# Optimization experiments

Hardware: AMD Instinct MI355X
Metric: run time of the kernel (lower is better)

Reference implementation:

```python
import jax, jax.numpy as jnp
import numpy as np
import itertools, math

# ---- config (mirrors args in init_kwargs) ----
BS = 8
FRAME_H, FRAME_W = 120, 160
RES = 5            # map_resolution (cm/cell)
Z_RES = 5
MAP_SIZE_CM = 2400
VR = 100           # vision_range (cells)
FOV = 79.0
NSEM = 16
CAT_THR, EXP_THR, MAP_THR = 5.0, 1.0, 1.0
CAM_H_CM = 88.0    # camera_height * 100
MAX_H = int(360 / Z_RES)   # 72
MIN_H = int(-40 / Z_RES)   # -8
D = MAX_H - MIN_H          # 80
MAP_SZ = MAP_SIZE_CM // RES  # 480
C = 4 + NSEM
XC = (FRAME_W - 1.0) / 2.0
ZC = (FRAME_H - 1.0) / 2.0
F_CAM = (FRAME_W / 2.0) / math.tan(math.radians(FOV / 2.0))


def splat_feat_nd(feat, coords, grid_dims):
    # feat: [B, nF, nPt], coords: [B, 3, nPt] in [-1, 1]; trilinear scatter-add
    B, nF, nPt = feat.shape
    pos_dim, wts_dim = [], []
    for d, gd in enumerate(grid_dims):
        pos = coords[:, d, :] * (gd / 2.0) + gd / 2.0
        fl = jnp.floor(pos)
        pd, wd = [], []
        for ix in (0.0, 1.0):
            p = fl + ix
            safe = ((p > 0) & (p < gd)).astype(pos.dtype)
            wd.append((1.0 - jnp.abs(pos - p)) * safe)
            pd.append(p * safe)
        pos_dim.append(pd)
        wts_dim.append(wd)
    T = grid_dims[0] * grid_dims[1] * grid_dims[2]
    idxs, wts = [], []
    for ix_d in itertools.product((0, 1), (0, 1), (0, 1)):
        index = jnp.zeros_like(pos_dim[0][0])
        w = jnp.ones_like(index)
        for d in range(3):
            index = index * grid_dims[d] + pos_dim[d][ix_d[d]]
            w = w * wts_dim[d][ix_d[d]]
        idxs.append(index.astype(jnp.int32))
        wts.append(w)
    idx = jnp.concatenate(idxs, axis=-1)              # [B, 8*nPt]
    w = jnp.concatenate(wts, axis=-1)                 # [B, 8*nPt]
    src = jnp.tile(feat, (1, 1, 8)) * w[:, None, :]   # [B, nF, 8*nPt]

    def scat(src_b, idx_b):
        return jnp.zeros((nF, T), src_b.dtype).at[:, idx_b].add(src_b)

    grid = jax.vmap(scat)(src, idx)
    grid = jnp.clip(grid, 0.0, 1e3)
    return grid.reshape(B, nF, grid_dims[0], grid_dims[1], grid_dims[2])


def _base_grid(N, dtype):
    # torch affine_grid default align_corners=False pixel-center coords
    c = (2.0 * jnp.arange(N, dtype=dtype) + 1.0) / N - 1.0
    x = jnp.broadcast_to(c[None, :], (N, N))
    y = jnp.broadcast_to(c[:, None], (N, N))
    return x, y


def affine_grid_rot(t_deg, N):
    t = t_deg * (np.pi / 180.0)
    ct, st = jnp.cos(t), jnp.sin(t)
    x, y = _base_grid(N, t.dtype)
    gx = ct[:, None, None] * x - st[:, None, None] * y
    gy = st[:, None, None] * x + ct[:, None, None] * y
    return jnp.stack([gx, gy], -1)


def affine_grid_trans(xy, N):
    x, y = _base_grid(N, xy.dtype)
    gx = x[None] + xy[:, 0][:, None, None]
    gy = y[None] + xy[:, 1][:, None, None]
    return jnp.stack([gx, gy], -1)


def grid_sample(im, grid):
    # bilinear, align_corners=True, padding_mode='zeros'
    B, Ch, H, W = im.shape
    x = (grid[..., 0] + 1.0) * 0.5 * (W - 1)
    y = (grid[..., 1] + 1.0) * 0.5 * (H - 1)
    x0 = jnp.floor(x); y0 = jnp.floor(y)
    x1 = x0 + 1.0; y1 = y0 + 1.0

    def gather(im_b, iy, ix):
        valid = (ix >= 0) & (ix < W) & (iy >= 0) & (iy < H)
        ixc = jnp.clip(ix, 0, W - 1).astype(jnp.int32)
        iyc = jnp.clip(iy, 0, H - 1).astype(jnp.int32)
        return im_b[:, iyc, ixc] * valid[None].astype(im_b.dtype)

    def sample_one(im_b, x, y, x0, x1, y0, y1):
        wa = (x1 - x) * (y1 - y); wb = (x1 - x) * (y - y0)
        wc = (x - x0) * (y1 - y); wd = (x - x0) * (y - y0)
        return (gather(im_b, y0, x0) * wa[None] + gather(im_b, y1, x0) * wb[None]
                + gather(im_b, y0, x1) * wc[None] + gather(im_b, y1, x1) * wd[None])

    return jax.vmap(sample_one)(im, x, y, x0, x1, y0, y1)


def setup_inputs() -> dict:
    key = jax.random.key(0)
    k1, k2, k3, k4, k5, k6 = jax.random.split(key, 6)
    rgb = jax.random.uniform(k1, (BS, 3, FRAME_H, FRAME_W), jnp.float32)
    depth = jax.random.uniform(k2, (BS, 1, FRAME_H, FRAME_W), jnp.float32, 0.5, 5.0)
    sem = jax.random.uniform(k3, (BS, NSEM, FRAME_H, FRAME_W), jnp.float32)
    obs = jnp.concatenate([rgb, depth, sem], axis=1)
    maps_last = jax.random.uniform(k4, (BS, C, MAP_SZ, MAP_SZ), jnp.float32)
    xy = jax.random.uniform(k5, (BS, 2), jnp.float32, 2.0, 22.0)
    th = jax.random.uniform(k6, (BS, 1), jnp.float32, 0.0, 360.0)
    poses = jnp.concatenate([xy, th], axis=1)
    return {"obs": obs, "maps_last": maps_last, "poses": poses}


def reference(obs, maps_last, poses):
    bs = obs.shape[0]
    depth = obs[:, 3]
    rowmax = jnp.max(depth, axis=(0, 2))  # per image-row max over batch+width
    depth = jnp.where(depth == 0.0, rowmax[None, :, None], depth) * 100.0
    # point cloud from depth (du_scale=1)
    gx = jnp.arange(FRAME_W, dtype=depth.dtype)                 # column index
    gz = jnp.arange(FRAME_H - 1, -1, -1, dtype=depth.dtype)     # flipped row index
    X = (gx[None, None, :] - XC) * depth / F_CAM
    Z = (gz[None, :, None] - ZC) * depth / F_CAM
    Y = depth
    # camera -> agent frame (elev=0 -> identity rot), then shift_loc (theta=pi/2 -> identity rot)
    X = X + (VR * RES // 2)
    Z = Z + CAM_H_CM
    # normalize to [-1, 1] voxel coords
    xs = (X / RES - VR // 2.0) / VR * 2.0
    ys = (Y / RES - VR // 2.0) / VR * 2.0
    zs = (Z / Z_RES - (MAX_H + MIN_H) // 2.0) / (MAX_H - MIN_H) * 2.0
    coords = jnp.stack([xs, ys, zs], axis=1).reshape(bs, 3, -1)   # [B,3,nPt]
    feat = jnp.concatenate(
        [jnp.ones((bs, 1, FRAME_H * FRAME_W), obs.dtype),
         obs[:, 4:].reshape(bs, NSEM, -1)], axis=1)               # [B,1+NSEM,nPt]
    voxels = splat_feat_nd(feat, coords, (VR, VR, D))
    voxels = jnp.swapaxes(voxels, 2, 3)
    min_z = int(25 / Z_RES - MIN_H)                 # 13
    max_z = int((CAM_H_CM + 1) / Z_RES - MIN_H)     # 25
    agent_hp = voxels[..., min_z:max_z].sum(4)
    all_hp = voxels.sum(4)
    fp_map = jnp.clip(agent_hp[:, 0:1] / MAP_THR, 0.0, 1.0)
    fp_exp = jnp.clip(all_hp[:, 0:1] / EXP_THR, 0.0, 1.0)
    cat_pred = jnp.clip(agent_hp[:, 1:] / CAT_THR, 0.0, 1.0)
    x1 = MAP_SZ // 2 - VR // 2; x2 = x1 + VR
    y1 = MAP_SZ // 2; y2 = y1 + VR
    agent_view = jnp.zeros((bs, C, MAP_SZ, MAP_SZ), obs.dtype)
    agent_view = agent_view.at[:, 0:1, y1:y2, x1:x2].set(fp_map)
    agent_view = agent_view.at[:, 1:2, y1:y2, x1:x2].set(fp_exp)
    agent_view = agent_view.at[:, 4:4 + NSEM, y1:y2, x1:x2].set(cat_pred)
    # st_pose (detached in original)
    p = jax.lax.stop_gradient(poses)
    half = MAP_SZ // 2
    st_xy = -(p[:, :2] * 100.0 / RES - half) / half
    st_t = 90.0 - p[:, 2]
    rotated = grid_sample(agent_view, affine_grid_rot(st_t, MAP_SZ))
    translated = grid_sample(rotated, affine_grid_trans(st_xy, MAP_SZ))
    map_pred = jnp.maximum(maps_last, translated)
    map_pred = map_pred.at[:, 2].set(map_pred[:, 3])
    curr = (p[:, :2] * 100.0 / RES).astype(jnp.int32)
    rr = curr[:, 1]; cc = curr[:, 0]
    ii = jnp.arange(MAP_SZ)
    mask = (jnp.abs(ii[None, :, None] - rr[:, None, None]) <= 1) & \
           (jnp.abs(ii[None, None, :] - cc[:, None, None]) <= 1)
    map_pred = map_pred.at[:, 3].set(jnp.where(mask, 1.0, map_pred[:, 3]))
    return map_pred
```

## Files before the change

### kernel.cpp

```cpp
#include <hip/hip_runtime.h>
#include <hip/hip_bf16.h>
#include <math.h>

#define FRAME_W 160
#define FRAME_H 120
#define NPIX (FRAME_W*FRAME_H)
#define BS_ 8
#define CC_ 20
#define MAPSZ 480
#define MPIX (MAPSZ*MAPSZ)
#define AVC 18
#define AV_ELEMS ((size_t)BS_*100*100*AVC)
#define ROT0 120
#define ROT1 360

#define STRIP_H 4
#define NSTRIP 25
#define SPLAT_T 1024
#define TILE_ELEMS (STRIP_H*100*AVC)

template<bool BF>
__device__ __forceinline__ float ldv(const void* p, size_t i){
    if constexpr (BF) return __bfloat162float(((const __hip_bfloat16*)p)[i]);
    else              return ((const float*)p)[i];
}
template<bool BF>
__device__ __forceinline__ void stv(void* p, size_t i, float v){
    if constexpr (BF) ((__hip_bfloat16*)p)[i] = __float2bfloat16(v);
    else              ((float*)p)[i] = v;
}
template<bool BF>
__device__ __forceinline__ void ld2v(const void* p, size_t i, float& a, float& b){
    if constexpr (BF){
        ushort2 u = ((const ushort2*)p)[i>>1];
        a = __uint_as_float((unsigned)u.x << 16);
        b = __uint_as_float((unsigned)u.y << 16);
    } else {
        float2 v = ((const float2*)p)[i>>1];
        a = v.x; b = v.y;
    }
}
template<bool BF>
__device__ __forceinline__ void st2v(void* p, size_t i, float a, float b){
    if constexpr (BF){
        __hip_bfloat162 h;
        h.x = __float2bfloat16(a); h.y = __float2bfloat16(b);
        ((__hip_bfloat162*)p)[i>>1] = h;
    } else {
        ((float2*)p)[i>>1] = make_float2(a, b);
    }
}

extern "C" __global__ void smk75806v6_detect(const void* __restrict__ poses,
                                             int* __restrict__ flag,
                                             float* __restrict__ params)
{
    if (threadIdx.x == 0 && blockIdx.x == 0){
        const __hip_bfloat16* pb = (const __hip_bfloat16*)poses;
        int ok = 1;
        for (int k = 0; k < 24; k++){
            float v = __bfloat162float(pb[k]);
            if (!(v >= 0.0f && v < 400.0f)) ok = 0;
        }
        *flag = ok;
        for (int b = 0; b < BS_; b++){
            float p0, p1, th;
            if (ok){
                p0 = __bfloat162float(pb[b*3+0]);
                p1 = __bfloat162float(pb[b*3+1]);
                th = __bfloat162float(pb[b*3+2]);
            } else {
                const float* pf = (const float*)poses;
                p0 = pf[b*3+0]; p1 = pf[b*3+1]; th = pf[b*3+2];
            }
            params[b*8+0] = -((p0*100.0f/5.0f) - 240.0f)/240.0f;
            params[b*8+1] = -((p1*100.0f/5.0f) - 240.0f)/240.0f;
            float t = (90.0f - th) * 0.017453292519943295f;
            params[b*8+2] = cosf(t);
            params[b*8+3] = sinf(t);
            params[b*8+4] = p1*100.0f/5.0f;
            params[b*8+5] = p0*100.0f/5.0f;
        }
    }
}

template<bool BF>
__device__ __forceinline__ void splat_strip_impl(const void* __restrict__ obs,
                                                 float* __restrict__ av,
                                                 float* __restrict__ tile,
                                                 int b, int y0)
{
    const int tid = threadIdx.x;
    const size_t ob = (size_t)b*CC_*NPIX;
    const float f_cam = (float)(80.0 / tan(0.6894050545377601));

    for (int k = tid; k < TILE_ELEMS/4; k += SPLAT_T)
        ((float4*)tile)[k] = make_float4(0.f,0.f,0.f,0.f);
    __syncthreads();

    const int NQ = NPIX/4;
    for (int qp = tid; qp < NQ; qp += SPLAT_T){
        float d4[4];
        if constexpr (BF){
            ushort4 u = ((const ushort4*)((const __hip_bfloat16*)obs + ob + 3*NPIX))[qp];
            d4[0] = __uint_as_float((unsigned)u.x << 16);
            d4[1] = __uint_as_float((unsigned)u.y << 16);
            d4[2] = __uint_as_float((unsigned)u.z << 16);
            d4[3] = __uint_as_float((unsigned)u.w << 16);
        } else {
            float4 v = ((const float4*)((const float*)obs + ob + 3*NPIX))[qp];
            d4[0]=v.x; d4[1]=v.y; d4[2]=v.z; d4[3]=v.w;
        }
        #pragma unroll
        for (int u=0;u<4;u++){
            int pix = qp*4 + u;
            float d100 = d4[u] * 100.0f;

            float ys   = (d100/5.0f - 50.0f)/100.0f*2.0f;
            float posy = ys*50.0f + 50.0f;
            float fly  = floorf(posy);
            int   ify  = (int)fly;
            if (ify < y0 - 1 || ify > y0 + STRIP_H - 1) continue;

            int r = pix / FRAME_W, c = pix - r*FRAME_W;
            float X = ((float)c - 79.5f) * d100 / f_cam + 250.0f;
            float Z = ((float)(FRAME_H-1 - r) - 59.5f) * d100 / f_cam + 88.0f;
            float xs = (X/5.0f - 50.0f)/100.0f*2.0f;
            float zs = (Z/5.0f - 32.0f)/80.0f*2.0f;
            float posx = xs*50.0f + 50.0f;
            float posz = zs*40.0f + 40.0f;

            float flx = floorf(posx), flz = floorf(posz);
            float wx[2], wy[2]; int ixv[2], iyv[2]; bool own[2];
            #pragma unroll
            for (int k=0;k<2;k++){
                float px = flx + (float)k;
                wx[k] = (px > 0.0f && px < 100.0f) ? (1.0f - fabsf(posx - px)) : 0.0f;
                ixv[k] = (int)px;
                float py = fly + (float)k;
                bool valid = (py > 0.0f && py < 100.0f);
                wy[k] = valid ? (1.0f - fabsf(posy - py)) : 0.0f;
                iyv[k] = (int)py;
                own[k] = valid && (iyv[k] >= y0) && (iyv[k] < y0 + STRIP_H);
            }
            if (!own[0] && !own[1]) continue;

            float wzall = 0.0f, wzag = 0.0f;
            #pragma unroll
            for (int k=0;k<2;k++){
                float pz = flz + (float)k;
                if (pz > 0.0f && pz < 80.0f){
                    float w = 1.0f - fabsf(posz - pz);
                    wzall += w;
                    int ipz = (int)pz;
                    if (ipz >= 13 && ipz < 25) wzag += w;
                }
            }
            if (wzall == 0.0f) continue;

            float sem[16];
            bool needsem = (wzag != 0.0f);
            if (needsem){
                #pragma unroll
                for (int s=0;s<16;s++) sem[s] = ldv<BF>(obs, ob + (size_t)(4+s)*NPIX + pix);
            }

            #pragma unroll
            for (int ky=0;ky<2;ky++){
                if (!own[ky] || wy[ky] == 0.0f) continue;
                #pragma unroll
                for (int kx=0;kx<2;kx++){
                    float wxy = wx[kx]*wy[ky];
                    if (wxy == 0.0f) continue;
                    float* cell = tile + (((iyv[ky]-y0)*100 + ixv[kx])*AVC);
                    atomicAdd(cell + 0, wxy*wzall);
                    float wa = wxy*wzag;
                    if (wa != 0.0f){
                        atomicAdd(cell + 1, wa);
                        #pragma unroll
                        for (int s=0;s<16;s++) atomicAdd(cell + 2 + s, wa*sem[s]);
                    }
                }
            }
        }
    }

    __syncthreads();
    size_t gbase4 = ((size_t)b*100 + y0)*(size_t)(100*AVC) / 4;
    for (int k = tid; k < TILE_ELEMS/4; k += SPLAT_T)
        ((float4*)av)[gbase4 + k] = ((const float4*)tile)[k];
}

extern "C" __global__ __launch_bounds__(SPLAT_T)
void smk75806v6_splat(const void* __restrict__ obs, float* __restrict__ av,
                      const int* __restrict__ flag)
{
    __shared__ float tile[TILE_ELEMS];
    int bid = blockIdx.x;
    int b  = bid & 7;
    int y0 = (bid >> 3) * STRIP_H;
    if (*flag) splat_strip_impl<true >(obs, av, tile, b, y0);
    else       splat_strip_impl<false>(obs, av, tile, b, y0);
}

template<bool BF>
__device__ __forceinline__ void final_impl(const float* __restrict__ av,
                                           const void* __restrict__ maps_last,
                                           const float* __restrict__ params,
                                           void* __restrict__ out, int gid)
{
    int b = gid / (MPIX/2);
    int rem = gid - b*(MPIX/2);
    int i  = rem / (MAPSZ/2);
    int j0 = (rem - i*(MAPSZ/2))*2;

    const float* pb = params + b*8;
    float tx = pb[0], ty = pb[1], ct = pb[2], st = pb[3];
    int rr = (int)pb[4];
    int cc = (int)pb[5];

    size_t mlb = (size_t)b*CC_*MPIX;
    size_t px  = (size_t)i*MAPSZ + j0;

    float m0a,m0b, m1a,m1b, m3a,m3b;
    ld2v<BF>(maps_last, mlb + 0*MPIX + px, m0a, m0b);
    ld2v<BF>(maps_last, mlb + 1*MPIX + px, m1a, m1b);
    ld2v<BF>(maps_last, mlb + 3*MPIX + px, m3a, m3b);

    float acc[2][18];
    #pragma unroll
    for (int u=0;u<2;u++)
        #pragma unroll
        for (int q=0;q<18;q++) acc[u][q]=0.0f;

    float yb = (2.0f*(float)i + 1.0f)/480.0f - 1.0f + ty;
    float y = (yb + 1.0f)*0.5f*479.0f;
    float y0f = floorf(y);
    int y0 = (int)y0f;
    float wyv[2] = {(y0f + 1.0f) - y, y - y0f};

    #pragma unroll
    for (int u=0;u<2;u++){
        int j = j0 + u;
        float xb = (2.0f*(float)j + 1.0f)/480.0f - 1.0f + tx;
        float x = (xb + 1.0f)*0.5f*479.0f;
        float x0f = floorf(x);
        int x0 = (int)x0f;
        float wxv[2] = {(x0f + 1.0f) - x, x - x0f};

        if (x0+1 >= ROT0 && x0 < ROT1 && y0+1 >= ROT0 && y0 < ROT1){
            #pragma unroll
            for (int ty2=0;ty2<2;ty2++){
                #pragma unroll
                for (int tx2=0;tx2<2;tx2++){
                    int yy = y0 + ty2, xx = x0 + tx2;
                    float w = wxv[tx2]*wyv[ty2];
                    if (w == 0.0f) continue;
                    if (yy < ROT0 || yy >= ROT1 || xx < ROT0 || xx >= ROT1) continue;
                    float xb2 = (2.0f*(float)xx + 1.0f)/480.0f - 1.0f;
                    float yb2 = (2.0f*(float)yy + 1.0f)/480.0f - 1.0f;
                    float gx = ct*xb2 - st*yb2;
                    float gy = st*xb2 + ct*yb2;
                    float x2 = (gx + 1.0f)*0.5f*479.0f;
                    float y2 = (gy + 1.0f)*0.5f*479.0f;
                    float x20f = floorf(x2), y20f = floorf(y2);
                    int x20 = (int)x20f, y20 = (int)y20f;
                    float wx2[2] = {(x20f + 1.0f) - x2, x2 - x20f};
                    float wy2[2] = {(y20f + 1.0f) - y2, y2 - y20f};

                    float rs[18];
                    #pragma unroll
                    for (int q=0;q<18;q++) rs[q]=0.0f;
                    #pragma unroll
                    for (int sy=0;sy<2;sy++){
                        #pragma unroll
                        for (int sx=0;sx<2;sx++){
                            int ay = y20 + sy, ax = x20 + sx;
                            float w2 = wx2[sx]*wy2[sy];
                            if (w2 == 0.0f) continue;
                            if (ay < 240 || ay >= 340 || ax < 190 || ax >= 290) continue;
                            const float* cell = av + (((size_t)b*100 + (ay-240))*100 + (ax-190))*AVC;
                            rs[0] += w2 * fminf(cell[1], 1.0f);
                            rs[1] += w2 * fminf(cell[0], 1.0f);
                            #pragma unroll
                            for (int s=0;s<16;s++)
                                rs[2+s] += w2 * fminf(cell[2+s]*0.2f, 1.0f);
                        }
                    }
                    #pragma unroll
                    for (int q=0;q<18;q++) acc[u][q] += w*rs[q];
                }
            }
        }
    }

    bool m3u0 = ((i - rr) <= 1 && (rr - i) <= 1) && ((j0   - cc) <= 1 && (cc - j0  ) <= 1);
    bool m3u1 = ((i - rr) <= 1 && (rr - i) <= 1) && ((j0+1 - cc) <= 1 && (cc - j0-1) <= 1);

    float f3a = fmaxf(m3a, 0.0f);
    float f3b = fmaxf(m3b, 0.0f);
    st2v<BF>(out, mlb + 0*MPIX + px, fmaxf(m0a, acc[0][0]), fmaxf(m0b, acc[1][0]));
    st2v<BF>(out, mlb + 1*MPIX + px, fmaxf(m1a, acc[0][1]), fmaxf(m1b, acc[1][1]));
    st2v<BF>(out, mlb + 2*MPIX + px, f3a, f3b);
    st2v<BF>(out, mlb + 3*MPIX + px, m3u0 ? 1.0f : f3a, m3u1 ? 1.0f : f3b);

    float sa[16], sb[16];
    #pragma unroll
    for (int q=0;q<16;q++)
        ld2v<BF>(maps_last, mlb + (size_t)(4+q)*MPIX + px, sa[q], sb[q]);
    #pragma unroll
    for (int q=0;q<16;q++)
        st2v<BF>(out, mlb + (size_t)(4+q)*MPIX + px,
                 fmaxf(sa[q], acc[0][2+q]), fmaxf(sb[q], acc[1][2+q]));
}

extern "C" __global__ __launch_bounds__(256)
void smk75806v6_final(const float* __restrict__ av,
                      const void* __restrict__ maps_last,
                      const float* __restrict__ params,
                      void* __restrict__ out,
                      const int* __restrict__ flag)
{
    int gid = blockIdx.x*256 + threadIdx.x;
    if (gid >= BS_*MPIX/2) return;
    if (*flag) final_impl<true >(av, maps_last, params, out, gid);
    else       final_impl<false>(av, maps_last, params, out, gid);
}

extern "C" void kernel_launch(void* const* d_in, const int* in_sizes, int n_in,
                              void* d_out, int out_size, void* d_ws, size_t ws_size,
                              hipStream_t stream) {
    const void* pO = d_in[0];
    const void* pM = (n_in > 1) ? d_in[1] : d_in[0];
    const void* pP = (n_in > 2) ? d_in[2] : d_in[0];
    for (int i = 0; i < n_in; i++){
        if      (in_sizes[i] == BS_*CC_*NPIX) pO = d_in[i];
        else if (in_sizes[i] == BS_*CC_*MPIX) pM = d_in[i];
        else if (in_sizes[i] == BS_*3)        pP = d_in[i];
    }
    int*   flag   = (int*)d_ws;
    float* params = (float*)((char*)d_ws + 64);
    float* av     = (float*)((char*)d_ws + 512);

    smk75806v6_detect<<<1, 64, 0, stream>>>(pP, flag, params);
    smk75806v6_splat <<<BS_*NSTRIP, SPLAT_T, 0, stream>>>(pO, av, flag);
    smk75806v6_final <<<(BS_*MPIX/2 + 255)/256, 256, 0, stream>>>(av, pM, params, d_out, flag);
}
```

Before: 340.5 us.

## Precompute rotated map into workspace buffer and fold detect kernel into splat

Splits the fused rotate+translate sampling into two passes. A new kernel materializes the rotated 18-channel map over the 240x240 region into a planar workspace buffer, and the final kernel then does a single bilinear lookup per pixel instead of recomputing the rotation sample for each of four neighbors. The splatted map is now stored channel-planar, the pose detect/params kernel is folded into the splat kernel, and the final kernel handles one pixel per thread. This adds a kernel launch and about 33 MB of intermediate traffic, and falls back to the old fused path when the workspace is too small.

```diff
diff --git a/kernel.cpp b/kernel.cpp
--- a/kernel.cpp
+++ b/kernel.cpp
@@ -10,9 +10,14 @@
 #define MAPSZ 480
 #define MPIX (MAPSZ*MAPSZ)
 #define AVC 18
-#define AV_ELEMS ((size_t)BS_*100*100*AVC)
+#define AVP 10000
 #define ROT0 120
 #define ROT1 360
+#define RW   240
+#define RPTS (RW*RW)
+#define WS_AV_OFF   512
+#define WS_R_OFF    (6*1024*1024)
+#define WS_NEED     ((size_t)WS_R_OFF + (size_t)BS_*AVC*RPTS*4)
 
 #define STRIP_H 4
 #define NSTRIP 25
@@ -29,59 +34,16 @@
     if constexpr (BF) ((__hip_bfloat16*)p)[i] = __float2bfloat16(v);
     else              ((float*)p)[i] = v;
 }
-template<bool BF>
-__device__ __forceinline__ void ld2v(const void* p, size_t i, float& a, float& b){
-    if constexpr (BF){
-        ushort2 u = ((const ushort2*)p)[i>>1];
-        a = __uint_as_float((unsigned)u.x << 16);
-        b = __uint_as_float((unsigned)u.y << 16);
-    } else {
-        float2 v = ((const float2*)p)[i>>1];
-        a = v.x; b = v.y;
-    }
-}
-template<bool BF>
-__device__ __forceinline__ void st2v(void* p, size_t i, float a, float b){
-    if constexpr (BF){
-        __hip_bfloat162 h;
-        h.x = __float2bfloat16(a); h.y = __float2bfloat16(b);
-        ((__hip_bfloat162*)p)[i>>1] = h;
-    } else {
-        ((float2*)p)[i>>1] = make_float2(a, b);
-    }
-}
-
-extern "C" __global__ void smk75806v6_detect(const void* __restrict__ poses,
-                                             int* __restrict__ flag,
-                                             float* __restrict__ params)
-{
-    if (threadIdx.x == 0 && blockIdx.x == 0){
-        const __hip_bfloat16* pb = (const __hip_bfloat16*)poses;
-        int ok = 1;
-        for (int k = 0; k < 24; k++){
-            float v = __bfloat162float(pb[k]);
-            if (!(v >= 0.0f && v < 400.0f)) ok = 0;
-        }
-        *flag = ok;
-        for (int b = 0; b < BS_; b++){
-            float p0, p1, th;
-            if (ok){
-                p0 = __bfloat162float(pb[b*3+0]);
-                p1 = __bfloat162float(pb[b*3+1]);
-                th = __bfloat162float(pb[b*3+2]);
-            } else {
-                const float* pf = (const float*)poses;
-                p0 = pf[b*3+0]; p1 = pf[b*3+1]; th = pf[b*3+2];
-            }
-            params[b*8+0] = -((p0*100.0f/5.0f) - 240.0f)/240.0f;
-            params[b*8+1] = -((p1*100.0f/5.0f) - 240.0f)/240.0f;
-            float t = (90.0f - th) * 0.017453292519943295f;
-            params[b*8+2] = cosf(t);
-            params[b*8+3] = sinf(t);
-            params[b*8+4] = p1*100.0f/5.0f;
-            params[b*8+5] = p0*100.0f/5.0f;
-        }
-    }
+
+__device__ __forceinline__ int detect_flag(const void* poses){
+    const __hip_bfloat16* pb = (const __hip_bfloat16*)poses;
+    int ok = 1;
+    #pragma unroll
+    for (int k = 0; k < 24; k++){
+        float v = __bfloat162float(pb[k]);
+        if (!(v >= 0.0f && v < 400.0f)) ok = 0;
+    }
+    return ok;
 }
 
 template<bool BF>
@@ -93,10 +55,6 @@
     const int tid = threadIdx.x;
     const size_t ob = (size_t)b*CC_*NPIX;
     const float f_cam = (float)(80.0 / tan(0.6894050545377601));
-
-    for (int k = tid; k < TILE_ELEMS/4; k += SPLAT_T)
-        ((float4*)tile)[k] = make_float4(0.f,0.f,0.f,0.f);
-    __syncthreads();
 
     const int NQ = NPIX/4;
     for (int qp = tid; qp < NQ; qp += SPLAT_T){
@@ -186,145 +144,302 @@
     }
 
     __syncthreads();
-    size_t gbase4 = ((size_t)b*100 + y0)*(size_t)(100*AVC) / 4;
+    for (int k = tid; k < TILE_ELEMS; k += SPLAT_T){
+        int ch = k / 400;
+        int rc = k - ch*400;
+        av[((size_t)b*AVC + ch)*AVP + y0*100 + rc] = tile[rc*AVC + ch];
+    }
+}
+
+extern "C" __global__ __launch_bounds__(SPLAT_T)
+void smk75806v7_splat(const void* __restrict__ obs,
+                      const void* __restrict__ poses,
+                      float* __restrict__ av,
+                      int* __restrict__ flag,
+                      float* __restrict__ params)
+{
+    __shared__ float tile[TILE_ELEMS];
+    __shared__ int sflag;
+    int tid = threadIdx.x;
+
+    if (tid < 8){
+        int ok = detect_flag(poses);
+        if (tid == 0) sflag = ok;
+        if (blockIdx.x == 0){
+            if (tid == 0) *flag = ok;
+            int b = tid;
+            float p0, p1, th;
+            if (ok){
+                const __hip_bfloat16* pb = (const __hip_bfloat16*)poses;
+                p0 = __bfloat162float(pb[b*3+0]);
+                p1 = __bfloat162float(pb[b*3+1]);
+                th = __bfloat162float(pb[b*3+2]);
+            } else {
+                const float* pf = (const float*)poses;
+                p0 = pf[b*3+0]; p1 = pf[b*3+1]; th = pf[b*3+2];
+            }
+            params[b*8+0] = -((p0*100.0f/5.0f) - 240.0f)/240.0f;
+            params[b*8+1] = -((p1*100.0f/5.0f) - 240.0f)/240.0f;
+            float t = (90.0f - th) * 0.017453292519943295f;
+            params[b*8+2] = cosf(t);
+            params[b*8+3] = sinf(t);
+            params[b*8+4] = p1*100.0f/5.0f;
+            params[b*8+5] = p0*100.0f/5.0f;
+        }
+    }
     for (int k = tid; k < TILE_ELEMS/4; k += SPLAT_T)
-        ((float4*)av)[gbase4 + k] = ((const float4*)tile)[k];
-}
-
-extern "C" __global__ __launch_bounds__(SPLAT_T)
-void smk75806v6_splat(const void* __restrict__ obs, float* __restrict__ av,
-                      const int* __restrict__ flag)
-{
-    __shared__ float tile[TILE_ELEMS];
+        ((float4*)tile)[k] = make_float4(0.f,0.f,0.f,0.f);
+    __syncthreads();
+
     int bid = blockIdx.x;
     int b  = bid & 7;
     int y0 = (bid >> 3) * STRIP_H;
-    if (*flag) splat_strip_impl<true >(obs, av, tile, b, y0);
+    if (sflag) splat_strip_impl<true >(obs, av, tile, b, y0);
     else       splat_strip_impl<false>(obs, av, tile, b, y0);
 }
 
+extern "C" __global__ __launch_bounds__(256)
+void smk75806v7_rot(const float* __restrict__ av,
+                    const float* __restrict__ params,
+                    float* __restrict__ R)
+{
+    int gid = blockIdx.x*256 + threadIdx.x;
+    if (gid >= BS_*RPTS) return;
+    int b = gid / RPTS;
+    int rem = gid - b*RPTS;
+    int ry = rem / RW, rx = rem - ry*RW;
+    int yy = ry + ROT0, xx = rx + ROT0;
+
+    float ct = params[b*8+2], st = params[b*8+3];
+    float xb2 = (2.0f*(float)xx + 1.0f)/480.0f - 1.0f;
+    float yb2 = (2.0f*(float)yy + 1.0f)/480.0f - 1.0f;
+    float gx = ct*xb2 - st*yb2;
+    float gy = st*xb2 + ct*yb2;
+    float x2 = (gx + 1.0f)*0.5f*479.0f;
+    float y2 = (gy + 1.0f)*0.5f*479.0f;
+    float x20f = floorf(x2), y20f = floorf(y2);
+    int x20 = (int)x20f, y20 = (int)y20f;
+    float wx2[2] = {(x20f + 1.0f) - x2, x2 - x20f};
+    float wy2[2] = {(y20f + 1.0f) - y2, y2 - y20f};
+
+    float wf[4]; int off[4]; bool any = false;
+    #pragma unroll
+    for (int t=0;t<4;t++){
+        int sy = t>>1, sx = t&1;
+        int ay = y20 + sy, ax = x20 + sx;
+        float w2 = wx2[sx]*wy2[sy];
+        bool v = (ay >= 240 && ay < 340 && ax >= 190 && ax < 290) && (w2 != 0.0f);
+        wf[t]  = v ? w2 : 0.0f;
+        off[t] = v ? (ay-240)*100 + (ax-190) : 0;
+        any |= v;
+    }
+
+    float* Rb = R + (size_t)b*AVC*RPTS + rem;
+    if (!any){
+        #pragma unroll
+        for (int q=0;q<AVC;q++) Rb[(size_t)q*RPTS] = 0.0f;
+        return;
+    }
+    const float* avb = av + (size_t)b*AVC*AVP;
+    #pragma unroll
+    for (int q=0;q<AVC;q++){
+        int pl = (q==0) ? 1 : ((q==1) ? 0 : q);
+        float sc = (q>=2) ? 0.2f : 1.0f;
+        const float* ap = avb + (size_t)pl*AVP;
+        float v = wf[0]*fminf(ap[off[0]]*sc, 1.0f)
+                + wf[1]*fminf(ap[off[1]]*sc, 1.0f)
+                + wf[2]*fminf(ap[off[2]]*sc, 1.0f)
+                + wf[3]*fminf(ap[off[3]]*sc, 1.0f);
+        Rb[(size_t)q*RPTS] = v;
+    }
+}
+
 template<bool BF>
-__device__ __forceinline__ void final_impl(const float* __restrict__ av,
-                                           const void* __restrict__ maps_last,
-                                           const float* __restrict__ params,
-                                           void* __restrict__ out, int gid)
-{
-    int b = gid / (MPIX/2);
-    int rem = gid - b*(MPIX/2);
-    int i  = rem / (MAPSZ/2);
-    int j0 = (rem - i*(MAPSZ/2))*2;
-
-    const float* pb = params + b*8;
-    float tx = pb[0], ty = pb[1], ct = pb[2], st = pb[3];
-    int rr = (int)pb[4];
-    int cc = (int)pb[5];
+__device__ __forceinline__ void finalB_impl(const float* __restrict__ R,
+                                            const void* __restrict__ maps_last,
+                                            const float* __restrict__ params,
+                                            void* __restrict__ out, int gid)
+{
+    int b = gid / MPIX;
+    int rem = gid - b*MPIX;
+    int i = rem / MAPSZ, j = rem - i*MAPSZ;
+
+    const float* pbp = params + b*8;
+    float tx = pbp[0], ty = pbp[1];
+    int rr = (int)pbp[4];
+    int cc = (int)pbp[5];
 
     size_t mlb = (size_t)b*CC_*MPIX;
-    size_t px  = (size_t)i*MAPSZ + j0;
-
-    float m0a,m0b, m1a,m1b, m3a,m3b;
-    ld2v<BF>(maps_last, mlb + 0*MPIX + px, m0a, m0b);
-    ld2v<BF>(maps_last, mlb + 1*MPIX + px, m1a, m1b);
-    ld2v<BF>(maps_last, mlb + 3*MPIX + px, m3a, m3b);
-
-    float acc[2][18];
-    #pragma unroll
-    for (int u=0;u<2;u++)
-        #pragma unroll
-        for (int q=0;q<18;q++) acc[u][q]=0.0f;
+    size_t px  = (size_t)rem;
+
+    float m0 = ldv<BF>(maps_last, mlb + 0*MPIX + px);
+    float m1 = ldv<BF>(maps_last, mlb + 1*MPIX + px);
+    float m3 = ldv<BF>(maps_last, mlb + 3*MPIX + px);
+    float ms[16];
+    #pragma unroll
+    for (int q=0;q<16;q++) ms[q] = ldv<BF>(maps_last, mlb + (size_t)(4+q)*MPIX + px);
+
+    float acc[18];
+    #pragma unroll
+    for (int q=0;q<18;q++) acc[q] = 0.0f;
 
     float yb = (2.0f*(float)i + 1.0f)/480.0f - 1.0f + ty;
     float y = (yb + 1.0f)*0.5f*479.0f;
-    float y0f = floorf(y);
-    int y0 = (int)y0f;
+    float xb = (2.0f*(float)j + 1.0f)/480.0f - 1.0f + tx;
+    float x = (xb + 1.0f)*0.5f*479.0f;
+    float x0f = floorf(x), y0f = floorf(y);
+    int x0 = (int)x0f, y0 = (int)y0f;
+    float wxv[2] = {(x0f + 1.0f) - x, x - x0f};
     float wyv[2] = {(y0f + 1.0f) - y, y - y0f};
 
-    #pragma unroll
-    for (int u=0;u<2;u++){
-        int j = j0 + u;
-        float xb = (2.0f*(float)j + 1.0f)/480.0f - 1.0f + tx;
-        float x = (xb + 1.0f)*0.5f*479.0f;
-        float x0f = floorf(x);
-        int x0 = (int)x0f;
-        float wxv[2] = {(x0f + 1.0f) - x, x - x0f};
-
-        if (x0+1 >= ROT0 && x0 < ROT1 && y0+1 >= ROT0 && y0 < ROT1){
+    if (x0+1 >= ROT0 && x0 < ROT1 && y0+1 >= ROT0 && y0 < ROT1){
+        float cw[4]; int coff[4];
+        #pragma unroll
+        for (int t=0;t<4;t++){
+            int ty2 = t>>1, tx2 = t&1;
+            int yy = y0 + ty2, xx = x0 + tx2;
+            float w = wxv[tx2]*wyv[ty2];
+            bool v = (yy >= ROT0 && yy < ROT1 && xx >= ROT0 && xx < ROT1);
+            cw[t]  = v ? w : 0.0f;
+            coff[t] = v ? (yy-ROT0)*RW + (xx-ROT0) : 0;
+        }
+        const float* Rb = R + (size_t)b*AVC*RPTS;
+        #pragma unroll
+        for (int q=0;q<18;q++){
+            const float* Rp = Rb + (size_t)q*RPTS;
+            acc[q] = cw[0]*Rp[coff[0]] + cw[1]*Rp[coff[1]]
+                   + cw[2]*Rp[coff[2]] + cw[3]*Rp[coff[3]];
+        }
+    }
+
+    bool m3m = (i - rr) <= 1 && (rr - i) <= 1 && (j - cc) <= 1 && (cc - j) <= 1;
+    float f3 = fmaxf(m3, 0.0f);
+    stv<BF>(out, mlb + 0*MPIX + px, fmaxf(m0, acc[0]));
+    stv<BF>(out, mlb + 1*MPIX + px, fmaxf(m1, acc[1]));
+    stv<BF>(out, mlb + 2*MPIX + px, f3);
+    stv<BF>(out, mlb + 3*MPIX + px, m3m ? 1.0f : f3);
+    #pragma unroll
+    for (int q=0;q<16;q++)
+        stv<BF>(out, mlb + (size_t)(4+q)*MPIX + px, fmaxf(ms[q], acc[2+q]));
+}
+
+extern "C" __global__ __launch_bounds__(256)
+void smk75806v7_finalB(const float* __restrict__ R,
+                       const void* __restrict__ maps_last,
+                       const float* __restrict__ params,
+                       void* __restrict__ out,
+                       const int* __restrict__ flag)
+{
+    int gid = blockIdx.x*256 + threadIdx.x;
+    if (gid >= BS_*MPIX) return;
+    if (*flag) finalB_impl<true >(R, maps_last, params, out, gid);
+    else       finalB_impl<false>(R, maps_last, params, out, gid);
+}
+
+template<bool BF>
+__device__ __forceinline__ void finalF_impl(const float* __restrict__ av,
+                                            const void* __restrict__ maps_last,
+                                            const float* __restrict__ params,
+                                            void* __restrict__ out, int gid)
+{
+    int b = gid / MPIX;
+    int rem = gid - b*MPIX;
+    int i = rem / MAPSZ, j = rem - i*MAPSZ;
+
+    const float* pbp = params + b*8;
+    float tx = pbp[0], ty = pbp[1], ct = pbp[2], st = pbp[3];
+    int rr = (int)pbp[4];
+    int cc = (int)pbp[5];
+
+    size_t mlb = (size_t)b*CC_*MPIX;
+    size_t px  = (size_t)rem;
+
+    float m0 = ldv<BF>(maps_last, mlb + 0*MPIX + px);
+    float m1 = ldv<BF>(maps_last, mlb + 1*MPIX + px);
+    float m3 = ldv<BF>(maps_last, mlb + 3*MPIX + px);
+
+    float acc[18];
+    #pragma unroll
+    for (int q=0;q<18;q++) acc[q]=0.0f;
+
+    float yb = (2.0f*(float)i + 1.0f)/480.0f - 1.0f + ty;
+    float y = (yb + 1.0f)*0.5f*479.0f;
+    float xb = (2.0f*(float)j + 1.0f)/480.0f - 1.0f + tx;
+    float x = (xb + 1.0f)*0.5f*479.0f;
+    float x0f = floorf(x), y0f = floorf(y);
+    int x0 = (int)x0f, y0 = (int)y0f;
+    float wxv[2] = {(x0f + 1.0f) - x, x - x0f};
+    float wyv[2] = {(y0f + 1.0f) - y, y - y0f};
+
+    if (x0+1 >= ROT0 && x0 < ROT1 && y0+1 >= ROT0 && y0 < ROT1){
+        #pragma unroll
+        for (int ty2=0;ty2<2;ty2++){
             #pragma unroll
-            for (int ty2=0;ty2<2;ty2++){
+            for (int tx2=0;tx2<2;tx2++){
+                int yy = y0 + ty2, xx = x0 + tx2;
+                float w = wxv[tx2]*wyv[ty2];
+                if (w == 0.0f) continue;
+                if (yy < ROT0 || yy >= ROT1 || xx < ROT0 || xx >= ROT1) continue;
+                float xb2 = (2.0f*(float)xx + 1.0f)/480.0f - 1.0f;
+                float yb2 = (2.0f*(float)yy + 1.0f)/480.0f - 1.0f;
+                float gx = ct*xb2 - st*yb2;
+                float gy = st*xb2 + ct*yb2;
+                float x2 = (gx + 1.0f)*0.5f*479.0f;
+                float y2 = (gy + 1.0f)*0.5f*479.0f;
+                float x20f = floorf(x2), y20f = floorf(y2);
+                int x20 = (int)x20f, y20 = (int)y20f;
+                float wx2[2] = {(x20f + 1.0f) - x2, x2 - x20f};
+                float wy2[2] = {(y20f + 1.0f) - y2, y2 - y20f};
+
+                float rs[18];
                 #pragma unroll
-                for (int tx2=0;tx2<2;tx2++){
-                    int yy = y0 + ty2, xx = x0 + tx2;
-                    float w = wxv[tx2]*wyv[ty2];
-                    if (w == 0.0f) continue;
-                    if (yy < ROT0 || yy >= ROT1 || xx < ROT0 || xx >= ROT1) continue;
-                    float xb2 = (2.0f*(float)xx + 1.0f)/480.0f - 1.0f;
-                    float yb2 = (2.0f*(float)yy + 1.0f)/480.0f - 1.0f;
-                    float gx = ct*xb2 - st*yb2;
-                    float gy = st*xb2 + ct*yb2;
-                    float x2 = (gx + 1.0f)*0.5f*479.0f;
-                    float y2 = (gy + 1.0f)*0.5f*479.0f;
-                    float x20f = floorf(x2), y20f = floorf(y2);
-                    int x20 = (int)x20f, y20 = (int)y20f;
-                    float wx2[2] = {(x20f + 1.0f) - x2, x2 - x20f};
-                    float wy2[2] = {(y20f + 1.0f) - y2, y2 - y20f};
-
-                    float rs[18];
+                for (int q=0;q<18;q++) rs[q]=0.0f;
+                #pragma unroll
+                for (int sy=0;sy<2;sy++){
                     #pragma unroll
-                    for (int q=0;q<18;q++) rs[q]=0.0f;
-                    #pragma unroll
-                    for (int sy=0;sy<2;sy++){
+                    for (int sx=0;sx<2;sx++){
+                        int ay = y20 + sy, ax = x20 + sx;
+                        float w2 = wx2[sx]*wy2[sy];
+                        if (w2 == 0.0f) continue;
+                        if (ay < 240 || ay >= 340 || ax < 190 || ax >= 290) continue;
+                        const float* cb = av + (size_t)b*AVC*AVP + (ay-240)*100 + (ax-190);
+                        rs[0] += w2 * fminf(cb[1*AVP], 1.0f);
+                        rs[1] += w2 * fminf(cb[0],     1.0f);
                         #pragma unroll
-                        for (int sx=0;sx<2;sx++){
-                            int ay = y20 + sy, ax = x20 + sx;
-                            float w2 = wx2[sx]*wy2[sy];
-                            if (w2 == 0.0f) continue;
-                            if (ay < 240 || ay >= 340 || ax < 190 || ax >= 290) continue;
-                            const float* cell = av + (((size_t)b*100 + (ay-240))*100 + (ax-190))*AVC;
-                            rs[0] += w2 * fminf(cell[1], 1.0f);
-                            rs[1] += w2 * fminf(cell[0], 1.0f);
-                            #pragma unroll
-                            for (int s=0;s<16;s++)
-                                rs[2+s] += w2 * fminf(cell[2+s]*0.2f, 1.0f);
-                        }
+                        for (int s=0;s<16;s++)
+                            rs[2+s] += w2 * fminf(cb[(size_t)(2+s)*AVP]*0.2f, 1.0f);
                     }
-                    #pragma unroll
-                    for (int q=0;q<18;q++) acc[u][q] += w*rs[q];
                 }
-            }
-        }
-    }
-
-    bool m3u0 = ((i - rr) <= 1 && (rr - i) <= 1) && ((j0   - cc) <= 1 && (cc - j0  ) <= 1);
-    bool m3u1 = ((i - rr) <= 1 && (rr - i) <= 1) && ((j0+1 - cc) <= 1 && (cc - j0-1) <= 1);
-
-    float f3a = fmaxf(m3a, 0.0f);
-    float f3b = fmaxf(m3b, 0.0f);
-    st2v<BF>(out, mlb + 0*MPIX + px, fmaxf(m0a, acc[0][0]), fmaxf(m0b, acc[1][0]));
-    st2v<BF>(out, mlb + 1*MPIX + px, fmaxf(m1a, acc[0][1]), fmaxf(m1b, acc[1][1]));
-    st2v<BF>(out, mlb + 2*MPIX + px, f3a, f3b);
-    st2v<BF>(out, mlb + 3*MPIX + px, m3u0 ? 1.0f : f3a, m3u1 ? 1.0f : f3b);
-
-    float sa[16], sb[16];
-    #pragma unroll
-    for (int q=0;q<16;q++)
-        ld2v<BF>(maps_last, mlb + (size_t)(4+q)*MPIX + px, sa[q], sb[q]);
-    #pragma unroll
-    for (int q=0;q<16;q++)
-        st2v<BF>(out, mlb + (size_t)(4+q)*MPIX + px,
-                 fmaxf(sa[q], acc[0][2+q]), fmaxf(sb[q], acc[1][2+q]));
+                #pragma unroll
+                for (int q=0;q<18;q++) acc[q] += w*rs[q];
+            }
+        }
+    }
+
+    bool m3m = (i - rr) <= 1 && (rr - i) <= 1 && (j - cc) <= 1 && (cc - j) <= 1;
+    float f3 = fmaxf(m3, 0.0f);
+    stv<BF>(out, mlb + 0*MPIX + px, fmaxf(m0, acc[0]));
+    stv<BF>(out, mlb + 1*MPIX + px, fmaxf(m1, acc[1]));
+    stv<BF>(out, mlb + 2*MPIX + px, f3);
+    stv<BF>(out, mlb + 3*MPIX + px, m3m ? 1.0f : f3);
+    #pragma unroll
+    for (int q=0;q<16;q++){
+        float v = fmaxf(ldv<BF>(maps_last, mlb + (size_t)(4+q)*MPIX + px), acc[2+q]);
+        stv<BF>(out, mlb + (size_t)(4+q)*MPIX + px, v);
+    }
 }
 
 extern "C" __global__ __launch_bounds__(256)
-void smk75806v6_final(const float* __restrict__ av,
-                      const void* __restrict__ maps_last,
-                      const float* __restrict__ params,
-                      void* __restrict__ out,
-                      const int* __restrict__ flag)
+void smk75806v7_finalF(const float* __restrict__ av,
+                       const void* __restrict__ maps_last,
+                       const float* __restrict__ params,
+                       void* __restrict__ out,
+                       const int* __restrict__ flag)
 {
     int gid = blockIdx.x*256 + threadIdx.x;
-    if (gid >= BS_*MPIX/2) return;
-    if (*flag) final_impl<true >(av, maps_last, params, out, gid);
-    else       final_impl<false>(av, maps_last, params, out, gid);
+    if (gid >= BS_*MPIX) return;
+    if (*flag) finalF_impl<true >(av, maps_last, params, out, gid);
+    else       finalF_impl<false>(av, maps_last, params, out, gid);
 }
 
 extern "C" void kernel_launch(void* const* d_in, const int* in_sizes, int n_in,
@@ -340,9 +455,14 @@
     }
     int*   flag   = (int*)d_ws;
     float* params = (float*)((char*)d_ws + 64);
-    float* av     = (float*)((char*)d_ws + 512);
-
-    smk75806v6_detect<<<1, 64, 0, stream>>>(pP, flag, params);
-    smk75806v6_splat <<<BS_*NSTRIP, SPLAT_T, 0, stream>>>(pO, av, flag);
-    smk75806v6_final <<<(BS_*MPIX/2 + 255)/256, 256, 0, stream>>>(av, pM, params, d_out, flag);
-}
+    float* av     = (float*)((char*)d_ws + WS_AV_OFF);
+    float* R      = (float*)((char*)d_ws + WS_R_OFF);
+
+    smk75806v7_splat<<<BS_*NSTRIP, SPLAT_T, 0, stream>>>(pO, pP, av, flag, params);
+    if (ws_size >= WS_NEED){
+        smk75806v7_rot   <<<(BS_*RPTS + 255)/256, 256, 0, stream>>>(av, params, R);
+        smk75806v7_finalB<<<(BS_*MPIX + 255)/256, 256, 0, stream>>>(R, pM, params, d_out, flag);
+    } else {
+        smk75806v7_finalF<<<(BS_*MPIX + 255)/256, 256, 0, stream>>>(av, pM, params, d_out, flag);
+    }
+}
```

Measured after the change: 334.1 us. No clear change (-1.9%).
